# Kernel tuning notes

Hardware: AMD Instinct MI355X
Metric: run time of the kernel (lower is better)

The kernel has to match this reference:

```python
import jax, jax.numpy as jnp
import numpy as np

ALPHA = 32.0 ** 2
HEADS = 8
DIM_HEAD = 64
EPS = 1e-5


def _leaky(x):
    return jnp.where(x >= 0, x, 0.1 * x)


def _cpb_bias(fmap_size, w0, b0, w1, b1, w2, b2):
    # continuous position bias: MLP over signed-log relative coords -> [h, n, n]
    pos = jnp.arange(fmap_size)
    gi, gj = jnp.meshgrid(pos, pos, indexing='ij')
    grid = jnp.stack([gi, gj], axis=-1).reshape(-1, 2)  # [n, 2]
    rel = grid[:, None, :] - grid[None, :, :]           # [n, n, 2]
    rel = jnp.sign(rel) * jnp.log(jnp.abs(rel) + 1.0)
    h = _leaky(jnp.einsum('ijc,dc->ijd', rel.astype(jnp.float32), w0) + b0)
    h = _leaky(jnp.einsum('ijc,dc->ijd', h, w1) + b1)
    h = jnp.einsum('ijc,hc->ijh', h, w2) + b2           # [n, n, heads]
    return jnp.transpose(h, (2, 0, 1))                  # [heads, n, n]


def _stable_softmax(t, alpha=ALPHA):
    t = t / alpha
    t = t - jax.lax.stop_gradient(jnp.max(t, axis=-1, keepdims=True))
    return jax.nn.softmax(t * alpha, axis=-1)


def setup_inputs() -> dict:
    key = jax.random.key(0)
    ks = jax.random.split(key, 9)
    B, C, H, W = 8, 512, 32, 32
    inner = HEADS * DIM_HEAD
    s = 0.05
    return {
        'x': jax.random.normal(ks[0], (B, C, H, W), jnp.float32),
        'gamma': jnp.ones((1, C, 1, 1), jnp.float32),
        'w_qkv': jax.random.normal(ks[1], (inner * 3, C), jnp.float32) * s,
        'w_out': jax.random.normal(ks[2], (C, inner), jnp.float32) * s,
        'cpb_w0': jax.random.normal(ks[3], (128, 2), jnp.float32) * s,
        'cpb_b0': jax.random.normal(ks[4], (128,), jnp.float32) * s,
        'cpb_w1': jax.random.normal(ks[5], (128, 128), jnp.float32) * s,
        'cpb_b1': jax.random.normal(ks[6], (128,), jnp.float32) * s,
        'cpb_w2': jax.random.normal(ks[7], (HEADS, 128), jnp.float32) * s,
        'cpb_b2': jax.random.normal(ks[8], (HEADS,), jnp.float32) * s,
    }


def reference(x, gamma, w_qkv, w_out, cpb_w0, cpb_b0, cpb_w1, cpb_b1, cpb_w2, cpb_b2):
    B, C, H, W = x.shape
    n = H * W
    scale = DIM_HEAD ** -0.5
    residual = x

    # LayerNormChan: normalize over channel dim with biased variance
    mean = jnp.mean(x, axis=1, keepdims=True)
    var = jnp.var(x, axis=1, keepdims=True)
    xn = (x - mean) / jnp.sqrt(var + EPS) * gamma

    # 1x1 conv qkv projection as matmul over channels
    xf = xn.reshape(B, C, n)                              # [B, C, n]
    qkv = jnp.einsum('oc,bcn->bon', w_qkv, xf)            # [B, 3*inner, n]
    q, k, v = jnp.split(qkv, 3, axis=1)
    rs = lambda t: t.reshape(B, HEADS, DIM_HEAD, n)
    q, k, v = rs(q), rs(k), rs(v)

    sim = jnp.einsum('bhdi,bhdj->bhij', q, k) * scale     # [B, h, n, n]
    bias = _cpb_bias(H, cpb_w0, cpb_b0, cpb_w1, cpb_b1, cpb_w2, cpb_b2)
    sim = sim + bias[None]

    attn = _stable_softmax(sim)
    out = jnp.einsum('bhij,bhdj->bhdi', attn, v)          # [B, h, d, n]
    out = out.reshape(B, HEADS * DIM_HEAD, n)
    out = jnp.einsum('oc,bcn->bon', w_out, out).reshape(B, C, H, W)
    return out + residual
```

## Files before the change

kernel.cpp:

```cpp
#include <hip/hip_runtime.h>
#include <hip/hip_bf16.h>

#define CCH   512
#define BATCH 8
#define NPOS  1024
#define MQKV  1536
#define EPS   1e-5f
#define LOG2E 1.4426950408889634f

typedef __attribute__((ext_vector_type(4))) float f32x4;
typedef __attribute__((ext_vector_type(8))) __bf16 bf16x8;
typedef __attribute__((ext_vector_type(8))) unsigned short u16x8;
typedef __attribute__((ext_vector_type(4))) unsigned short u16x4;

__device__ inline unsigned short f2bf(float f) {
  __hip_bfloat16 h = __float2bfloat16(f);
  return __builtin_bit_cast(unsigned short, h);
}
__device__ inline float bf2f(unsigned short u) {
  return __bfloat162float(__builtin_bit_cast(__hip_bfloat16, u));
}

__device__ inline int sw(int row, int col) { return row * 64 + (col ^ ((row & 7) << 3)); }
__device__ inline int swk(int row, int col) { return row * 64 + (col ^ (((row >> 2) & 7) << 3)); }
__device__ inline int sw32(int row, int lh) {
  return row * 32 + ((lh ^ ((row ^ (row >> 2)) & 3)) << 3);
}

__device__ inline void gload16(const void* g, void* l) {
  __builtin_amdgcn_global_load_lds((const __attribute__((address_space(1))) void*)g,
                                   (__attribute__((address_space(3))) void*)l, 16, 0, 0);
}

__global__ __launch_bounds__(256) void setup_kernel(
    const float* __restrict__ wq, const float* __restrict__ wo,
    unsigned short* __restrict__ wqb, unsigned short* __restrict__ wob,
    const float* __restrict__ x, const float* __restrict__ gamma,
    unsigned short* __restrict__ xnT,
    const float* __restrict__ table, unsigned short* __restrict__ biasP) {
  __shared__ float red[4][32][2];
  __shared__ float gsh[512];
  __shared__ unsigned short obuf[32 * 520];
  int bid = blockIdx.x, tid = threadIdx.x;

  if (bid >= 3328) {
    int base = ((bid - 3328) * 256 + tid) * 8;
    int h = base >> 20;
    int i = (base >> 10) & 1023;
    int j0 = base & 1023;
    int ib = i >> 5, il = i & 31;
    u16x8 outv;
    #pragma unroll
    for (int e = 0; e < 8; ++e) {
      int j = j0 + e;
      int dy = ib - (j >> 5) + 31;
      int dx = il - (j & 31) + 31;
      outv[e] = f2bf(table[h * 3969 + dy * 63 + dx]);
    }
    *(u16x8*)&biasP[base] = outv;
    return;
  }

  if (bid < 3072) {
    int i = bid * 256 + tid;
    if (i < MQKV * CCH) {
      float v = wq[i];
      if (i < 512 * CCH) v *= 0.125f * LOG2E;
      wqb[i] = f2bf(v);
    }
    if (i < CCH * CCH) wob[i] = f2bf(wo[i]);
  } else {
    int blk = bid - 3072;
    int b = blk >> 5, p0 = (blk & 31) * 32;
    int pl = tid & 31, wv = tid >> 6, cg = tid >> 5;
    gsh[tid] = gamma[tid];
    gsh[tid + 256] = gamma[tid + 256];
    const float* xp = x + (size_t)b * CCH * NPOS + p0 + pl;
    float vals[64];
    float s1 = 0.f, s2 = 0.f;
    #pragma unroll
    for (int j = 0; j < 64; ++j) {
      float v = xp[(size_t)(cg + 8 * j) * NPOS];
      vals[j] = v; s1 += v; s2 += v * v;
    }
    s1 += __shfl_xor(s1, 32, 64); s2 += __shfl_xor(s2, 32, 64);
    if ((tid & 63) < 32) { red[wv][pl][0] = s1; red[wv][pl][1] = s2; }
    __syncthreads();
    float t1 = 0.f, t2 = 0.f;
    #pragma unroll
    for (int w2i = 0; w2i < 4; ++w2i) { t1 += red[w2i][pl][0]; t2 += red[w2i][pl][1]; }
    float mean = t1 * (1.f / 512.f);
    float var = t2 * (1.f / 512.f) - mean * mean;
    float rstd = rsqrtf(var + EPS);
    #pragma unroll
    for (int j = 0; j < 64; ++j) {
      int c = cg + 8 * j;
      obuf[pl * 520 + c] = f2bf((vals[j] - mean) * rstd * gsh[c]);
    }
    __syncthreads();
    unsigned short* orow = xnT + ((size_t)b * NPOS + p0) * 512;
    #pragma unroll
    for (int i = 0; i < 8; ++i) {
      int c2 = tid + i * 256;
      int pp = c2 >> 6, ch = c2 & 63;
      *(u16x8*)&orow[(size_t)pp * 512 + ch * 8] = *(const u16x8*)&obuf[pp * 520 + ch * 8];
    }
  }
}

__global__ __launch_bounds__(256) void cpb_kernel(
    const float* __restrict__ w0, const float* __restrict__ b0,
    const float* __restrict__ w1, const float* __restrict__ b1,
    const float* __restrict__ w2, const float* __restrict__ b2,
    float* __restrict__ table) {
  __shared__ float w1s[128 * 129];
  __shared__ float w2s[8 * 128];
  __shared__ float sh1[2][128];
  __shared__ float sh2[2][128];
  int tid = threadIdx.x;
  #pragma unroll
  for (int i = 0; i < 64; ++i) {
    int idx = i * 256 + tid;
    w1s[(idx >> 7) * 129 + (idx & 127)] = w1[idx];
  }
  #pragma unroll
  for (int i = 0; i < 4; ++i) {
    int idx = i * 256 + tid;
    w2s[idx] = w2[idx];
  }
  int sub = tid >> 7, t = tid & 127;
  float w00 = w0[t * 2 + 0], w01 = w0[t * 2 + 1], bb0 = b0[t], bb1 = b1[t];
  int hh = t >> 4, k16 = t & 15;
  float b2h = b2[hh];
  __syncthreads();

  #pragma unroll 1
  for (int pass = 0; pass < 8; ++pass) {
    int d0 = (blockIdx.x * 8 + pass) * 2 + sub;
    bool ok = d0 < 3969;
    int d0c = ok ? d0 : 0;
    int dy = d0c / 63 - 31, dx = d0c % 63 - 31;
    float r0 = (dy > 0 ? 1.f : (dy < 0 ? -1.f : 0.f)) * logf(fabsf((float)dy) + 1.f);
    float r1 = (dx > 0 ? 1.f : (dx < 0 ? -1.f : 0.f)) * logf(fabsf((float)dx) + 1.f);
    float h0 = r0 * w00 + r1 * w01 + bb0;
    sh1[sub][t] = (h0 >= 0.f) ? h0 : 0.1f * h0;
    __syncthreads();
    float a = bb1;
    #pragma unroll 8
    for (int c = 0; c < 128; ++c) a += sh1[sub][c] * w1s[t * 129 + c];
    sh2[sub][t] = (a >= 0.f) ? a : 0.1f * a;
    __syncthreads();
    float o = 0.f;
    #pragma unroll
    for (int c = 0; c < 8; ++c) o += sh2[sub][k16 * 8 + c] * w2s[hh * 128 + k16 * 8 + c];
    #pragma unroll
    for (int mm = 1; mm < 16; mm <<= 1) o += __shfl_xor(o, mm, 64);
    if (k16 == 0 && ok) table[hh * 3969 + d0] = (o + b2h) * LOG2E;
    __syncthreads();
  }
}

__global__ __launch_bounds__(256) void gemm_qkv(const unsigned short* __restrict__ Ag,
                                                const unsigned short* __restrict__ Bg,
                                                unsigned short* __restrict__ qT,
                                                unsigned short* __restrict__ kT,
                                                unsigned short* __restrict__ vB) {
  __shared__ unsigned short smem[16384];
  int tid = threadIdx.x;
  int by = blockIdx.y;
  int m0 = by * 128, nn0 = blockIdx.x * 128;
  int wave = tid >> 6, lane = tid & 63;
  int wm = wave >> 1, wn = wave & 1;
  int l16 = lane & 15, lh = lane >> 4;
  int r4 = lane >> 2, c4 = lane & 3;
  int csw = ((c4 ^ (r4 & 3) ^ ((lane >> 4) & 3))) << 3;
  f32x4 acc[4][4];
  #pragma unroll
  for (int it = 0; it < 4; ++it)
    #pragma unroll
    for (int jt = 0; jt < 4; ++jt) acc[it][jt] = (f32x4){0.f, 0.f, 0.f, 0.f};

  #define GSTAGE(bsel, k0) do {                                                               \
    _Pragma("unroll")                                                                         \
    for (int i_ = 0; i_ < 2; ++i_) {                                                          \
      int grp_ = wave * 2 + i_;                                                               \
      int row_ = grp_ * 16 + r4;                                                              \
      gload16(&Ag[(size_t)(m0 + row_) * 512 + (k0) + csw], smem + (bsel) * 4096 + grp_ * 512);\
      gload16(&Bg[(size_t)(nn0 + row_) * 512 + (k0) + csw],                                   \
              smem + 8192 + (bsel) * 4096 + grp_ * 512);                                      \
    }                                                                                         \
  } while (0)

  GSTAGE(0, 0);
  __syncthreads();
  #pragma unroll 1
  for (int k = 0; k < 16; ++k) {
    if (k < 15) GSTAGE((k + 1) & 1, (k + 1) * 32);
    const unsigned short* As = smem + (k & 1) * 4096;
    const unsigned short* Bs = smem + 8192 + (k & 1) * 4096;
    bf16x8 a[4], b[4];
    #pragma unroll
    for (int it = 0; it < 4; ++it) a[it] = *(const bf16x8*)&As[sw32(wm * 64 + it * 16 + l16, lh)];
    #pragma unroll
    for (int jt = 0; jt < 4; ++jt) b[jt] = *(const bf16x8*)&Bs[sw32(wn * 64 + jt * 16 + l16, lh)];
    __builtin_amdgcn_s_setprio(1);
    #pragma unroll
    for (int it = 0; it < 4; ++it)
      #pragma unroll
      for (int jt = 0; jt < 4; ++jt)
        acc[it][jt] = __builtin_amdgcn_mfma_f32_16x16x32_bf16(a[it], b[jt], acc[it][jt], 0, 0, 0);
    __builtin_amdgcn_s_setprio(0);
    __syncthreads();
  }

  int sel = by >> 2;
  int hh0 = (by & 3) * 2;
  int bb = nn0 >> 10, p0 = nn0 & 1023;
  unsigned short* Cs = smem;
  if (sel < 2) {
    #pragma unroll
    for (int it = 0; it < 4; ++it)
      #pragma unroll
      for (int jt = 0; jt < 4; ++jt) {
        int nnl = wn * 64 + jt * 16 + l16;
        int mb = wm * 64 + it * 16 + lh * 4;
        #pragma unroll
        for (int r = 0; r < 4; ++r)
          Cs[nnl * 128 + ((mb + r) ^ ((nnl & 7) << 4))] = f2bf(acc[it][jt][r]);
      }
    __syncthreads();
    unsigned short* dst = (sel == 0) ? qT : kT;
    #pragma unroll
    for (int i = 0; i < 8; ++i) {
      int c = tid + i * 256;
      int hl = c >> 10, p = (c >> 3) & 127, ch = c & 7;
      int mb = hl * 64 + ch * 8;
      u16x8 val = *(u16x8*)&Cs[p * 128 + (mb ^ ((p & 7) << 4))];
      int bh = bb * 8 + hh0 + hl;
      *(u16x8*)&dst[((size_t)bh * 1024 + p0 + p) * 64 + ch * 8] = val;
    }
  } else {
    #pragma unroll
    for (int it = 0; it < 4; ++it)
      #pragma unroll
      for (int jt = 0; jt < 4; ++jt) {
        int nnl = wn * 64 + jt * 16 + l16;
        int mb = wm * 64 + it * 16 + lh * 4;
        #pragma unroll
        for (int r = 0; r < 4; ++r)
          Cs[(mb + r) * 128 + (nnl ^ (((mb + r) & 7) << 4))] = f2bf(acc[it][jt][r]);
      }
    __syncthreads();
    #pragma unroll
    for (int i = 0; i < 8; ++i) {
      int c = tid + i * 256;
      int mloc = c >> 4, ch = c & 15;
      u16x8 val = *(u16x8*)&Cs[mloc * 128 + ((ch * 8) ^ ((mloc & 7) << 4))];
      int d = mloc & 63, hl = mloc >> 6;
      int bh = bb * 8 + hh0 + hl;
      *(u16x8*)&vB[((size_t)bh * 64 + d) * 1024 + p0 + ch * 8] = val;
    }
  }
}

__global__ __launch_bounds__(256) void gemm_out(const unsigned short* __restrict__ Ag,
                                                const unsigned short* __restrict__ Bg,
                                                const float* __restrict__ xres,
                                                float* __restrict__ yout) {
  __shared__ unsigned short smem[12288];
  int tid = threadIdx.x;
  int m0 = blockIdx.y * 64, nn0 = blockIdx.x * 128;
  int wave = tid >> 6, lane = tid & 63;
  int wm = wave >> 1, wn = wave & 1;
  int l16 = lane & 15, lh = lane >> 4;
  int r4 = lane >> 2, c4 = lane & 3;
  int csw = ((c4 ^ (r4 & 3) ^ ((lane >> 4) & 3))) << 3;
  f32x4 acc[2][4];
  #pragma unroll
  for (int it = 0; it < 2; ++it)
    #pragma unroll
    for (int jt = 0; jt < 4; ++jt) acc[it][jt] = (f32x4){0.f, 0.f, 0.f, 0.f};

  #define OSTAGE(bsel, k0) do {                                                               \
    {                                                                                         \
      int row_ = wave * 16 + r4;                                                              \
      gload16(&Ag[(size_t)(m0 + row_) * 512 + (k0) + csw],                                    \
              smem + (bsel) * 2048 + wave * 512);                                             \
    }                                                                                         \
    _Pragma("unroll")                                                                         \
    for (int i_ = 0; i_ < 2; ++i_) {                                                          \
      int grp_ = wave * 2 + i_;                                                               \
      int row_ = grp_ * 16 + r4;                                                              \
      gload16(&Bg[(size_t)(nn0 + row_) * 512 + (k0) + csw],                                   \
              smem + 4096 + (bsel) * 4096 + grp_ * 512);                                      \
    }                                                                                         \
  } while (0)

  OSTAGE(0, 0);
  __syncthreads();
  #pragma unroll 1
  for (int k = 0; k < 16; ++k) {
    if (k < 15) OSTAGE((k + 1) & 1, (k + 1) * 32);
    const unsigned short* As = smem + (k & 1) * 2048;
    const unsigned short* Bs = smem + 4096 + (k & 1) * 4096;
    bf16x8 a[2], b[4];
    #pragma unroll
    for (int it = 0; it < 2; ++it) a[it] = *(const bf16x8*)&As[sw32(wm * 32 + it * 16 + l16, lh)];
    #pragma unroll
    for (int jt = 0; jt < 4; ++jt) b[jt] = *(const bf16x8*)&Bs[sw32(wn * 64 + jt * 16 + l16, lh)];
    __builtin_amdgcn_s_setprio(1);
    #pragma unroll
    for (int it = 0; it < 2; ++it)
      #pragma unroll
      for (int jt = 0; jt < 4; ++jt)
        acc[it][jt] = __builtin_amdgcn_mfma_f32_16x16x32_bf16(a[it], b[jt], acc[it][jt], 0, 0, 0);
    __builtin_amdgcn_s_setprio(0);
    __syncthreads();
  }

  #pragma unroll
  for (int it = 0; it < 2; ++it) {
    int mbase = m0 + wm * 32 + it * 16 + lh * 4;
    #pragma unroll
    for (int jt = 0; jt < 4; ++jt) {
      int nn = nn0 + wn * 64 + jt * 16 + l16;
      int bb = nn >> 10, p = nn & 1023;
      #pragma unroll
      for (int r = 0; r < 4; ++r) {
        size_t addr = ((size_t)bb * 512 + mbase + r) * 1024 + p;
        yout[addr] = acc[it][jt][r] + xres[addr];
      }
    }
  }
}

__global__ __launch_bounds__(512) void attn_kernel(const unsigned short* __restrict__ qT,
                                                   const unsigned short* __restrict__ kT,
                                                   const unsigned short* __restrict__ vB,
                                                   const unsigned short* __restrict__ biasP,
                                                   unsigned short* __restrict__ attnout) {
  __shared__ unsigned short Kbuf[2][64 * 64];
  __shared__ unsigned short Vbuf[2][64 * 64];
  __shared__ unsigned short Ps[8][16 * 64];
  int tid = threadIdx.x;
  int bh = blockIdx.x;
  int i0 = blockIdx.y * 128;
  int hh = bh & 7, bb = bh >> 3;
  int w = tid >> 6, lane = tid & 63, l16 = lane & 15, lh = lane >> 4;
  int rsub = lane >> 3, csub = lane & 7;
  int scswV = (csub ^ rsub) * 8;
  int scswK = (csub ^ ((w * 2 + (rsub >> 2)) & 7)) * 8;

  const unsigned short* kbase = kT + (size_t)bh * NPOS * 64;
  const unsigned short* vbase = vB + (size_t)bh * 64 * NPOS;
  const unsigned short* bptr  = biasP + ((size_t)hh * 1024 + i0 + w * 16) * 1024 + l16 * 4;

  int qrow = i0 + w * 16 + l16;
  const unsigned short* qb = qT + ((size_t)bh * NPOS + qrow) * 64 + lh * 8;
  bf16x8 qreg[2];
  qreg[0] = *(const bf16x8*)&qb[0];
  qreg[1] = *(const bf16x8*)&qb[32];

  f32x4 o[5];
  #pragma unroll
  for (int dt = 0; dt < 5; ++dt) o[dt] = (f32x4){0.f, 0.f, 0.f, 0.f};

  bf16x8 ones;
  {
    u16x8 tmp = {0x3F80, 0x3F80, 0x3F80, 0x3F80, 0x3F80, 0x3F80, 0x3F80, 0x3F80};
    ones = __builtin_bit_cast(bf16x8, tmp);
  }

  #define STAGE(Kd, Vd, jj) do {                                                        \
    gload16(&kbase[(size_t)((jj) + w * 8 + rsub) * 64 + scswK], &(Kd)[w * 512]);        \
    gload16(&vbase[(size_t)(w * 8 + rsub) * 1024 + (jj) + scswV], &(Vd)[w * 512]);      \
  } while (0)

  STAGE(Kbuf[0], Vbuf[0], 0);
  __syncthreads();

  #pragma unroll 1
  for (int t = 0; t < 16; ++t) {
    int j0 = t * 64;
    if (t < 15) STAGE(Kbuf[(t + 1) & 1], Vbuf[(t + 1) & 1], j0 + 64);

    const unsigned short* Ks = Kbuf[t & 1];
    const unsigned short* Vs = Vbuf[t & 1];

    u16x4 bv4[4];
    #pragma unroll
    for (int r = 0; r < 4; ++r) bv4[r] = *(const u16x4*)&bptr[(lh * 4 + r) * 1024 + j0];

    f32x4 s[4];
    #pragma unroll
    for (int jt = 0; jt < 4; ++jt) s[jt] = (f32x4){0.f, 0.f, 0.f, 0.f};
    __builtin_amdgcn_s_setprio(1);
    #pragma unroll
    for (int ks = 0; ks < 2; ++ks) {
      int koff = ks * 32 + lh * 8;
      #pragma unroll
      for (int jt = 0; jt < 4; ++jt) {
        bf16x8 bk = *(const bf16x8*)&Ks[swk(l16 * 4 + jt, koff)];
        s[jt] = __builtin_amdgcn_mfma_f32_16x16x32_bf16(qreg[ks], bk, s[jt], 0, 0, 0);
      }
    }
    __builtin_amdgcn_s_setprio(0);

    #pragma unroll
    for (int r = 0; r < 4; ++r) {
      int rloc = lh * 4 + r;
      u16x4 pq;
      #pragma unroll
      for (int jt = 0; jt < 4; ++jt)
        pq[jt] = f2bf(__builtin_amdgcn_exp2f(s[jt][r] + bf2f(bv4[r][jt])));
      *(u16x4*)&Ps[w][sw(rloc, l16 * 4)] = pq;
    }

    __builtin_amdgcn_s_setprio(1);
    #pragma unroll
    for (int js = 0; js < 2; ++js) {
      int koff = js * 32 + lh * 8;
      bf16x8 pa = *(const bf16x8*)&Ps[w][sw(l16, koff)];
      #pragma unroll
      for (int dt = 0; dt < 4; ++dt) {
        bf16x8 vb = *(const bf16x8*)&Vs[sw(dt * 16 + l16, koff)];
        o[dt] = __builtin_amdgcn_mfma_f32_16x16x32_bf16(pa, vb, o[dt], 0, 0, 0);
      }
      o[4] = __builtin_amdgcn_mfma_f32_16x16x32_bf16(pa, ones, o[4], 0, 0, 0);
    }
    __builtin_amdgcn_s_setprio(0);

    __syncthreads();
  }

  #pragma unroll
  for (int r = 0; r < 4; ++r) {
    float inv = 1.f / o[4][r];
    int gi = i0 + w * 16 + lh * 4 + r;
    #pragma unroll
    for (int dt = 0; dt < 4; ++dt)
      attnout[((size_t)bb * 1024 + gi) * 512 + hh * 64 + dt * 16 + l16] = f2bf(o[dt][r] * inv);
  }
}

extern "C" void kernel_launch(void* const* d_in, const int* in_sizes, int n_in,
                              void* d_out, int out_size, void* d_ws, size_t ws_size,
                              hipStream_t stream) {
  const float* x     = (const float*)d_in[0];
  const float* gamma = (const float*)d_in[1];
  const float* w_qkv = (const float*)d_in[2];
  const float* w_out = (const float*)d_in[3];
  const float* cw0   = (const float*)d_in[4];
  const float* cb0   = (const float*)d_in[5];
  const float* cw1   = (const float*)d_in[6];
  const float* cb1   = (const float*)d_in[7];
  const float* cw2   = (const float*)d_in[8];
  const float* cb2   = (const float*)d_in[9];
  float* out = (float*)d_out;

  char* ws = (char*)d_ws;
  unsigned short* xnT   = (unsigned short*)(ws + 0);
  unsigned short* wqb   = (unsigned short*)(ws + 8388608);
  unsigned short* wob   = (unsigned short*)(ws + 9961472);
  unsigned short* qT    = (unsigned short*)(ws + 10485760);
  unsigned short* kT    = (unsigned short*)(ws + 18874368);
  unsigned short* vB    = (unsigned short*)(ws + 27262976);
  float*          table = (float*)(ws + 35651584);
  unsigned short* biasP = (unsigned short*)(ws + 35782656);
  unsigned short* aout  = (unsigned short*)(ws + 52559872);

  cpb_kernel<<<256, 256, 0, stream>>>(cw0, cb0, cw1, cb1, cw2, cb2, table);
  setup_kernel<<<7424, 256, 0, stream>>>(w_qkv, w_out, wqb, wob, x, gamma, xnT, table, biasP);
  gemm_qkv<<<dim3(64, 12), 256, 0, stream>>>(wqb, xnT, qT, kT, vB);
  attn_kernel<<<dim3(64, 8), 512, 0, stream>>>(qT, kT, vB, biasP, aout);
  gemm_out<<<dim3(64, 8), 256, 0, stream>>>(wob, aout, x, out);
}
```

Measured before the change: 101.3 us.

## Triple-buffer LDS staging with partial vmcnt waits in GEMMs and attention

Converts the double-buffered global-to-LDS pipelines in the QKV GEMM, output GEMM and attention kernel to three-stage ring buffers that prefetch two tiles ahead. The full __syncthreads is replaced by an explicit s_waitcnt vmcnt(N) plus barrier, so loads for the newest stage can stay in flight across the barrier. This aims to hide more global-load latency, at the cost of extra LDS per block and therefore possibly lower occupancy. In attention, the bias loads are moved ahead of the stage issue, so the vmcnt accounting depends on how the compiler orders those loads.

```diff
diff --git a/kernel.cpp b/kernel.cpp
--- a/kernel.cpp
+++ b/kernel.cpp
@@ -31,6 +31,12 @@
   __builtin_amdgcn_global_load_lds((const __attribute__((address_space(1))) void*)g,
                                    (__attribute__((address_space(3))) void*)l, 16, 0, 0);
 }
+
+#define CBAR(N) do {                                              \
+    asm volatile("s_waitcnt vmcnt(" #N ")" ::: "memory");         \
+    asm volatile("s_waitcnt lgkmcnt(0)" ::: "memory");            \
+    __builtin_amdgcn_s_barrier();                                 \
+  } while (0)
 
 __global__ __launch_bounds__(256) void setup_kernel(
     const float* __restrict__ wq, const float* __restrict__ wo,
@@ -165,7 +171,7 @@
                                                 unsigned short* __restrict__ qT,
                                                 unsigned short* __restrict__ kT,
                                                 unsigned short* __restrict__ vB) {
-  __shared__ unsigned short smem[16384];
+  __shared__ unsigned short smem[24576];
   int tid = threadIdx.x;
   int by = blockIdx.y;
   int m0 = by * 128, nn0 = blockIdx.x * 128;
@@ -187,17 +193,21 @@
       int row_ = grp_ * 16 + r4;                                                              \
       gload16(&Ag[(size_t)(m0 + row_) * 512 + (k0) + csw], smem + (bsel) * 4096 + grp_ * 512);\
       gload16(&Bg[(size_t)(nn0 + row_) * 512 + (k0) + csw],                                   \
-              smem + 8192 + (bsel) * 4096 + grp_ * 512);                                      \
+              smem + 12288 + (bsel) * 4096 + grp_ * 512);                                     \
     }                                                                                         \
   } while (0)
 
   GSTAGE(0, 0);
-  __syncthreads();
+  GSTAGE(1, 32);
+  asm volatile("s_waitcnt vmcnt(4)" ::: "memory");
+  __builtin_amdgcn_s_barrier();
+  int cur = 0;
   #pragma unroll 1
   for (int k = 0; k < 16; ++k) {
-    if (k < 15) GSTAGE((k + 1) & 1, (k + 1) * 32);
-    const unsigned short* As = smem + (k & 1) * 4096;
-    const unsigned short* Bs = smem + 8192 + (k & 1) * 4096;
+    int stg = (cur == 0) ? 2 : cur - 1;
+    if (k < 14) GSTAGE(stg, (k + 2) * 32);
+    const unsigned short* As = smem + cur * 4096;
+    const unsigned short* Bs = smem + 12288 + cur * 4096;
     bf16x8 a[4], b[4];
     #pragma unroll
     for (int it = 0; it < 4; ++it) a[it] = *(const bf16x8*)&As[sw32(wm * 64 + it * 16 + l16, lh)];
@@ -210,7 +220,8 @@
       for (int jt = 0; jt < 4; ++jt)
         acc[it][jt] = __builtin_amdgcn_mfma_f32_16x16x32_bf16(a[it], b[jt], acc[it][jt], 0, 0, 0);
     __builtin_amdgcn_s_setprio(0);
-    __syncthreads();
+    if (k < 14) CBAR(4); else CBAR(0);
+    cur = (cur == 2) ? 0 : cur + 1;
   }
 
   int sel = by >> 2;
@@ -267,7 +278,7 @@
                                                 const unsigned short* __restrict__ Bg,
                                                 const float* __restrict__ xres,
                                                 float* __restrict__ yout) {
-  __shared__ unsigned short smem[12288];
+  __shared__ unsigned short smem[18432];
   int tid = threadIdx.x;
   int m0 = blockIdx.y * 64, nn0 = blockIdx.x * 128;
   int wave = tid >> 6, lane = tid & 63;
@@ -292,17 +303,21 @@
       int grp_ = wave * 2 + i_;                                                               \
       int row_ = grp_ * 16 + r4;                                                              \
       gload16(&Bg[(size_t)(nn0 + row_) * 512 + (k0) + csw],                                   \
-              smem + 4096 + (bsel) * 4096 + grp_ * 512);                                      \
+              smem + 6144 + (bsel) * 4096 + grp_ * 512);                                      \
     }                                                                                         \
   } while (0)
 
   OSTAGE(0, 0);
-  __syncthreads();
+  OSTAGE(1, 32);
+  asm volatile("s_waitcnt vmcnt(3)" ::: "memory");
+  __builtin_amdgcn_s_barrier();
+  int cur = 0;
   #pragma unroll 1
   for (int k = 0; k < 16; ++k) {
-    if (k < 15) OSTAGE((k + 1) & 1, (k + 1) * 32);
-    const unsigned short* As = smem + (k & 1) * 2048;
-    const unsigned short* Bs = smem + 4096 + (k & 1) * 4096;
+    int stg = (cur == 0) ? 2 : cur - 1;
+    if (k < 14) OSTAGE(stg, (k + 2) * 32);
+    const unsigned short* As = smem + cur * 2048;
+    const unsigned short* Bs = smem + 6144 + cur * 4096;
     bf16x8 a[2], b[4];
     #pragma unroll
     for (int it = 0; it < 2; ++it) a[it] = *(const bf16x8*)&As[sw32(wm * 32 + it * 16 + l16, lh)];
@@ -315,7 +330,8 @@
       for (int jt = 0; jt < 4; ++jt)
         acc[it][jt] = __builtin_amdgcn_mfma_f32_16x16x32_bf16(a[it], b[jt], acc[it][jt], 0, 0, 0);
     __builtin_amdgcn_s_setprio(0);
-    __syncthreads();
+    if (k < 14) CBAR(3); else CBAR(0);
+    cur = (cur == 2) ? 0 : cur + 1;
   }
 
   #pragma unroll
@@ -339,8 +355,8 @@
                                                    const unsigned short* __restrict__ vB,
                                                    const unsigned short* __restrict__ biasP,
                                                    unsigned short* __restrict__ attnout) {
-  __shared__ unsigned short Kbuf[2][64 * 64];
-  __shared__ unsigned short Vbuf[2][64 * 64];
+  __shared__ unsigned short Kbuf[3][64 * 64];
+  __shared__ unsigned short Vbuf[3][64 * 64];
   __shared__ unsigned short Ps[8][16 * 64];
   int tid = threadIdx.x;
   int bh = blockIdx.x;
@@ -377,19 +393,24 @@
   } while (0)
 
   STAGE(Kbuf[0], Vbuf[0], 0);
-  __syncthreads();
+  STAGE(Kbuf[1], Vbuf[1], 64);
+  asm volatile("s_waitcnt vmcnt(2)" ::: "memory");
+  __builtin_amdgcn_s_barrier();
+  int cur = 0;
 
   #pragma unroll 1
   for (int t = 0; t < 16; ++t) {
     int j0 = t * 64;
-    if (t < 15) STAGE(Kbuf[(t + 1) & 1], Vbuf[(t + 1) & 1], j0 + 64);
-
-    const unsigned short* Ks = Kbuf[t & 1];
-    const unsigned short* Vs = Vbuf[t & 1];
 
     u16x4 bv4[4];
     #pragma unroll
     for (int r = 0; r < 4; ++r) bv4[r] = *(const u16x4*)&bptr[(lh * 4 + r) * 1024 + j0];
+
+    int stg = (cur == 0) ? 2 : cur - 1;
+    if (t < 14) STAGE(Kbuf[stg], Vbuf[stg], j0 + 128);
+
+    const unsigned short* Ks = Kbuf[cur];
+    const unsigned short* Vs = Vbuf[cur];
 
     f32x4 s[4];
     #pragma unroll
@@ -430,7 +451,8 @@
     }
     __builtin_amdgcn_s_setprio(0);
 
-    __syncthreads();
+    if (t < 14) CBAR(2); else CBAR(0);
+    cur = (cur == 2) ? 0 : cur + 1;
   }
 
   #pragma unroll
```

After: 100.7 us. Within noise of the previous version (-0.6%).
